# Kernel tuning notes

Measured on AMD Instinct MI355X. Metric: run time of the kernel, lower is better.

The kernel has to match this reference:

```python
import jax, jax.numpy as jnp
import numpy as np

N = 100000   # nodes
E = 1600000  # edges
S = 4        # state_dimension
H = 64       # hidden_channels


def _gcn_conv(x, row, col, W, b):
    """PyG GCNConv: h = x @ W; add self-loops; symmetric deg^-1/2 norm; scatter-add; + bias."""
    n = x.shape[0]
    h = x @ W  # [N, out]
    loop = jnp.arange(n, dtype=row.dtype)
    r = jnp.concatenate([row, loop])  # sources (with self-loops)
    c = jnp.concatenate([col, loop])  # targets (with self-loops)
    deg = jax.ops.segment_sum(jnp.ones(r.shape[0], h.dtype), c, num_segments=n)
    dinv = jnp.where(deg > 0, jax.lax.rsqrt(deg), 0.0)
    norm = dinv[r] * dinv[c]                      # [E+N]
    msg = h[r] * norm[:, None]                    # gather + scale, [E+N, out]
    out = jax.ops.segment_sum(msg, c, num_segments=n)  # scatter-add
    return out + b


def setup_inputs() -> dict:
    key = jax.random.key(0)
    k1, k2, k3, k4 = jax.random.split(key, 4)
    x = jax.random.normal(k1, (N, S), dtype=jnp.float32)
    edge_index = jax.random.randint(k2, (2, E), 0, N, dtype=jnp.int32)
    # Glorot-ish init for the two GCNConv linear layers (+ zero bias, PyG default)
    W1 = jax.random.normal(k3, (S, H), dtype=jnp.float32) * (1.0 / np.sqrt(S))
    b1 = jnp.zeros((H,), jnp.float32)
    W2 = jax.random.normal(k4, (H, S), dtype=jnp.float32) * (1.0 / np.sqrt(H))
    b2 = jnp.zeros((S,), jnp.float32)
    return {"x": x, "edge_index": edge_index, "W1": W1, "b1": b1, "W2": W2, "b2": b2}


def reference(x, edge_index, W1, b1, W2, b2):
    row, col = edge_index[0], edge_index[1]
    h = _gcn_conv(x, row, col, W1, b1)
    h = jax.nn.relu(h)
    out = _gcn_conv(h, row, col, W2, b2)
    return out
```

## Files before the change

### kernel.cpp

```cpp
#include <hip/hip_runtime.h>


#define CSHIFT  10
#define CNODES  1024
#define EPB     4096
#define PTH     512
#define PERBLK  128
#define PBSHIFT 7
#define CAPC    18432
#define HCAP    9216
#define ANODES  128
#define ACAP    2432

__global__ void __launch_bounds__(PTH) k_part(
        const int* __restrict__ row, const int* __restrict__ col,
        int e, int Kc, int NB, int* __restrict__ cnt,
        unsigned* __restrict__ stripe) {
    __shared__ int cur[128];
    int t = threadIdx.x, bx = blockIdx.x;
    if (t < 128) cur[t] = 0;
    __syncthreads();
    int lo = bx * EPB;
    int cbuf[8], rbuf[8];
#pragma unroll
    for (int k = 0; k < 8; ++k) {
        int i = lo + t + k * PTH;
        if (i < e) { cbuf[k] = col[i]; rbuf[k] = row[i]; }
        else { cbuf[k] = -1; rbuf[k] = 0; }
    }
    size_t sbase = (size_t)bx * PERBLK;
    size_t bstride = (size_t)NB * PERBLK;
#pragma unroll
    for (int k = 0; k < 8; ++k) {
        int c = cbuf[k];
        if (c < 0) continue;
        int b = c >> CSHIFT;
        int j = atomicAdd(&cur[b], 1);
        if (j < PERBLK)
            stripe[(size_t)b * bstride + sbase + j] =
                ((unsigned)rbuf[k] << CSHIFT) | (unsigned)(c & (CNODES - 1));
    }
    __syncthreads();
    if (t < Kc) cnt[t * NB + bx] = min(cur[t], PERBLK);
}

__global__ void __launch_bounds__(1024) k_sortH(
        const int* __restrict__ cnt, const unsigned* __restrict__ stripe,
        unsigned* __restrict__ sortedg, int* __restrict__ rstart,
        int* __restrict__ mtot, const float4* __restrict__ x,
        float* __restrict__ dinv, float4* __restrict__ y, int n, int NB) {
    __shared__ int hist[CNODES];
    __shared__ int cur[512];
    __shared__ int cntl[512];
    __shared__ unsigned sorted[HCAP];
    __shared__ int wsum[16], wpre[16];
    __shared__ int lowsh, msh;
    int bh = blockIdx.x, b = bh >> 1, h = bh & 1;
    int t = threadIdx.x, lane = t & 63, wv = t >> 6;
    for (int i = t; i < NB; i += 1024) cntl[i] = cnt[b * NB + i];
    hist[t] = 0;
    __syncthreads();
    size_t s0 = (size_t)b * NB * PERBLK;
    int nslot4 = (NB * PERBLK) >> 2;
    const uint4* st4 = (const uint4*)(stripe + s0);
    for (int g = t; g < nslot4; g += 1024) {
        int slot = g << 2;
        int cb = cntl[slot >> PBSHIFT];
        int j = slot & (PERBLK - 1);
        if (j >= cb) continue;
        uint4 w = st4[g];
        atomicAdd(&hist[w.x & (CNODES - 1)], 1);
        if (j + 1 < cb) atomicAdd(&hist[w.y & (CNODES - 1)], 1);
        if (j + 2 < cb) atomicAdd(&hist[w.z & (CNODES - 1)], 1);
        if (j + 3 < cb) atomicAdd(&hist[w.w & (CNODES - 1)], 1);
    }
    __syncthreads();
    int hv = hist[t];
    int v = hv;
#pragma unroll
    for (int off = 1; off < 64; off <<= 1) {
        int u = __shfl_up(v, off);
        if (lane >= off) v += u;
    }
    if (lane == 63) wsum[wv] = v;
    __syncthreads();
    if (t < 16) {
        int s = 0;
        for (int i = 0; i < t; ++i) s += wsum[i];
        wpre[t] = s;
    }
    __syncthreads();
    int incl = v + wpre[wv];
    if (t == 511) lowsh = incl;
    if (t == 1023) msh = incl;
    __syncthreads();
    int st = incl - hv;
    int low = lowsh, m = msh;
    int base = h ? low : 0;
    if ((t >> 9) == h) {
        cur[t & 511] = st - base;
        rstart[(b << CSHIFT) + t] = b * CAPC + st;
        int node = (b << CSHIFT) + t;
        if (node < n) {
            float di = rsqrtf((float)hv + 1.0f);
            dinv[node] = di;
            float4 xv = x[node];
            y[node] = make_float4(xv.x * di, xv.y * di, xv.z * di, xv.w * di);
        }
    }
    if (t == 0 && h == 0) mtot[b] = m;
    __syncthreads();
    for (int g = t; g < nslot4; g += 1024) {
        int slot = g << 2;
        int cb = cntl[slot >> PBSHIFT];
        int j = slot & (PERBLK - 1);
        if (j >= cb) continue;
        uint4 w = st4[g];
        int l0 = w.x & (CNODES - 1);
        if ((l0 >> 9) == h) { int p = atomicAdd(&cur[l0 & 511], 1); if (p < HCAP) sorted[p] = w.x >> CSHIFT; }
        if (j + 1 < cb) { int l = w.y & (CNODES - 1);
            if ((l >> 9) == h) { int p = atomicAdd(&cur[l & 511], 1); if (p < HCAP) sorted[p] = w.y >> CSHIFT; } }
        if (j + 2 < cb) { int l = w.z & (CNODES - 1);
            if ((l >> 9) == h) { int p = atomicAdd(&cur[l & 511], 1); if (p < HCAP) sorted[p] = w.z >> CSHIFT; } }
        if (j + 3 < cb) { int l = w.w & (CNODES - 1);
            if ((l >> 9) == h) { int p = atomicAdd(&cur[l & 511], 1); if (p < HCAP) sorted[p] = w.w >> CSHIFT; } }
    }
    __syncthreads();
    int cown = h ? (m - low) : low;
    int wb = min(cown, HCAP);
    size_t d0 = (size_t)b * CAPC + base;
    for (int i = t; i < wb; i += 1024) sortedg[d0 + i] = sorted[i];
}

__global__ void __launch_bounds__(512) k_mid(
        const unsigned* __restrict__ ere, const int* __restrict__ rstart,
        const int* __restrict__ mtot, const float* __restrict__ dinv,
        const float4* __restrict__ x, const float4* __restrict__ y,
        const float* __restrict__ W1, const float* __restrict__ b1,
        const float* __restrict__ W2, const float* __restrict__ b2,
        float4* __restrict__ z, float4* __restrict__ out, int n) {
    __shared__ unsigned recs[ACAP];
    __shared__ float4 sums[ANODES];
    int g = blockIdx.x, t = threadIdx.x;
    int nlo = g * ANODES;
    int b = nlo >> CSHIFT;
    int s0 = rstart[nlo];
    int e0 = ((g & 7) == 7) ? b * CAPC + min(mtot[b], CAPC)
                            : rstart[nlo + ANODES];
    int len = min(e0 - s0, ACAP);
    for (int i = t; i < len; i += 512) recs[i] = ere[s0 + i];
    __syncthreads();
    int tt = t >> 2, q = t & 3;
    int s = rstart[nlo + tt] - s0;
    int epos = (tt == ANODES - 1) ? len : min(rstart[nlo + tt + 1] - s0, len);
    float vx = 0.f, vy = 0.f, vz = 0.f, vw = 0.f;
    int i = s + q;
    while (i + 12 < epos) {
        int r0 = recs[i], r1 = recs[i + 4], r2 = recs[i + 8], r3 = recs[i + 12];
        float4 a0 = y[r0], a1 = y[r1], a2 = y[r2], a3 = y[r3];
        vx += a0.x + a1.x + a2.x + a3.x;
        vy += a0.y + a1.y + a2.y + a3.y;
        vz += a0.z + a1.z + a2.z + a3.z;
        vw += a0.w + a1.w + a2.w + a3.w;
        i += 16;
    }
    for (; i < epos; i += 4) {
        float4 a = y[recs[i]];
        vx += a.x; vy += a.y; vz += a.z; vw += a.w;
    }
    vx += __shfl_xor(vx, 1); vx += __shfl_xor(vx, 2);
    vy += __shfl_xor(vy, 1); vy += __shfl_xor(vy, 2);
    vz += __shfl_xor(vz, 1); vz += __shfl_xor(vz, 2);
    vw += __shfl_xor(vw, 1); vw += __shfl_xor(vw, 2);
    if (q == 0) sums[tt] = make_float4(vx, vy, vz, vw);
    __syncthreads();
    int node = nlo + t;
    if (t < ANODES && node < n) {
        float di = dinv[node], sl = di * di;
        float4 sv = sums[t];
        float4 xv = x[node];
        float a0 = di * sv.x + xv.x * sl;
        float a1 = di * sv.y + xv.y * sl;
        float a2 = di * sv.z + xv.z * sl;
        float a3 = di * sv.w + xv.w * sl;
        float t0 = 0.f, t1 = 0.f, t2 = 0.f, t3 = 0.f;
#pragma unroll 8
        for (int j = 0; j < 64; ++j) {
            float hh = b1[j] + a0 * W1[j] + a1 * W1[64 + j] + a2 * W1[128 + j] + a3 * W1[192 + j];
            hh = fmaxf(hh, 0.f);
            t0 += hh * W2[j * 4 + 0];
            t1 += hh * W2[j * 4 + 1];
            t2 += hh * W2[j * 4 + 2];
            t3 += hh * W2[j * 4 + 3];
        }
        z[node] = make_float4(t0 * di, t1 * di, t2 * di, t3 * di);
        out[node] = make_float4(b2[0] + t0 * sl, b2[1] + t1 * sl,
                                b2[2] + t2 * sl, b2[3] + t3 * sl);
    }
}

__global__ void __launch_bounds__(512) k_acc2(
        const unsigned* __restrict__ ere, const int* __restrict__ rstart,
        const int* __restrict__ mtot, const float* __restrict__ dinv,
        const float4* __restrict__ z, float4* __restrict__ out, int n) {
    __shared__ unsigned recs[ACAP];
    __shared__ float4 sums[ANODES];
    int g = blockIdx.x, t = threadIdx.x;
    int nlo = g * ANODES;
    int b = nlo >> CSHIFT;
    int s0 = rstart[nlo];
    int e0 = ((g & 7) == 7) ? b * CAPC + min(mtot[b], CAPC)
                            : rstart[nlo + ANODES];
    int len = min(e0 - s0, ACAP);
    for (int i = t; i < len; i += 512) recs[i] = ere[s0 + i];
    __syncthreads();
    int tt = t >> 2, q = t & 3;
    int s = rstart[nlo + tt] - s0;
    int epos = (tt == ANODES - 1) ? len : min(rstart[nlo + tt + 1] - s0, len);
    float vx = 0.f, vy = 0.f, vz = 0.f, vw = 0.f;
    int i = s + q;
    while (i + 12 < epos) {
        int r0 = recs[i], r1 = recs[i + 4], r2 = recs[i + 8], r3 = recs[i + 12];
        float4 a0 = z[r0], a1 = z[r1], a2 = z[r2], a3 = z[r3];
        vx += a0.x + a1.x + a2.x + a3.x;
        vy += a0.y + a1.y + a2.y + a3.y;
        vz += a0.z + a1.z + a2.z + a3.z;
        vw += a0.w + a1.w + a2.w + a3.w;
        i += 16;
    }
    for (; i < epos; i += 4) {
        float4 a = z[recs[i]];
        vx += a.x; vy += a.y; vz += a.z; vw += a.w;
    }
    vx += __shfl_xor(vx, 1); vx += __shfl_xor(vx, 2);
    vy += __shfl_xor(vy, 1); vy += __shfl_xor(vy, 2);
    vz += __shfl_xor(vz, 1); vz += __shfl_xor(vz, 2);
    vw += __shfl_xor(vw, 1); vw += __shfl_xor(vw, 2);
    if (q == 0) sums[tt] = make_float4(vx, vy, vz, vw);
    __syncthreads();
    int node = nlo + t;
    if (t < ANODES && node < n) {
        float di = dinv[node];
        float4 sv = sums[t];
        float4 o = out[node];
        out[node] = make_float4(o.x + di * sv.x, o.y + di * sv.y,
                                o.z + di * sv.z, o.w + di * sv.w);
    }
}

extern "C" void kernel_launch(void* const* d_in, const int* in_sizes, int n_in,
                              void* d_out, int out_size, void* d_ws, size_t ws_size,
                              hipStream_t stream) {
    const float* x  = (const float*)d_in[0];
    const int* edge = (const int*)d_in[1];
    const float* W1 = (const float*)d_in[2];
    const float* b1 = (const float*)d_in[3];
    const float* W2 = (const float*)d_in[4];
    const float* b2 = (const float*)d_in[5];
    float* out = (float*)d_out;

    const int n = in_sizes[0] / 4;
    const int e = in_sizes[1] / 2;
    const int* row = edge;
    const int* col = edge + e;
    const int Kc = (n + CNODES - 1) >> CSHIFT;
    const int NB = (e + EPB - 1) / EPB;

    char* ws = (char*)d_ws;
    float* y    = (float*)ws;  ws += (size_t)4 * n * 4;
    float* zmid = (float*)ws;  ws += (size_t)4 * n * 4;
    float* dinv = (float*)ws;  ws += (size_t)n * 4;
    unsigned* stripe = (unsigned*)ws;  ws += (size_t)Kc * NB * PERBLK * 4;
    unsigned* sortedg = (unsigned*)ws; ws += (size_t)Kc * CAPC * 4;
    int* cnt    = (int*)ws;    ws += (size_t)Kc * NB * 4;
    int* rstart = (int*)ws;    ws += (size_t)Kc * CNODES * 4;
    int* mtot   = (int*)ws;    ws += (size_t)Kc * 4;

    const int ga = (n + ANODES - 1) / ANODES;

    k_part<<<NB, PTH, 0, stream>>>(row, col, e, Kc, NB, cnt, stripe);
    k_sortH<<<2 * Kc, 1024, 0, stream>>>(cnt, stripe, sortedg, rstart, mtot,
                                         (const float4*)x, dinv, (float4*)y,
                                         n, NB);
    k_mid<<<ga, 512, 0, stream>>>(sortedg, rstart, mtot, dinv, (const float4*)x,
                                  (const float4*)y, W1, b1, W2, b2,
                                  (float4*)zmid, (float4*)out, n);
    k_acc2<<<ga, 512, 0, stream>>>(sortedg, rstart, mtot, dinv,
                                   (const float4*)zmid, (float4*)out, n);
}
```

Baseline: 125.7 us.

## Split sort into quarter-bucket blocks, per-wave partition histograms, direct global edge reads

The partition kernel now builds per-wave histograms and prefix offsets before scattering, which cuts contention on shared atomics. Each stripe segment shrinks to 96 slots. The sort kernel is split into four 512-thread blocks per 1024-node bucket instead of two 1024-thread blocks. This doubles the grid and shrinks shared memory per block, but every block still rescans the whole stripe. The aggregation kernels drop the shared-memory staging of edge records and read sorted indices straight from global memory, which removes a sync and the ACAP truncation. The risk is more redundant stripe reads and less coalesced index loads.

Measured after the change: 135.6 us. 7.9% more time.

```diff
diff --git a/kernel.cpp b/kernel.cpp
--- a/kernel.cpp
+++ b/kernel.cpp
@@ -5,20 +5,20 @@
 #define CNODES  1024
 #define EPB     4096
 #define PTH     512
-#define PERBLK  128
-#define PBSHIFT 7
+#define PERBLK  96
+#define QPS     24
 #define CAPC    18432
-#define HCAP    9216
+#define QCAP    4608
 #define ANODES  128
-#define ACAP    2432
+#define NBMAX   512
 
 __global__ void __launch_bounds__(PTH) k_part(
         const int* __restrict__ row, const int* __restrict__ col,
         int e, int Kc, int NB, int* __restrict__ cnt,
         unsigned* __restrict__ stripe) {
-    __shared__ int cur[128];
-    int t = threadIdx.x, bx = blockIdx.x;
-    if (t < 128) cur[t] = 0;
+    __shared__ int wh[8][128];
+    int t = threadIdx.x, w = t >> 6, bx = blockIdx.x;
+    for (int k = t; k < 8 * 128; k += PTH) ((int*)wh)[k] = 0;
     __syncthreads();
     int lo = bx * EPB;
     int cbuf[8], rbuf[8];
@@ -28,55 +28,69 @@
         if (i < e) { cbuf[k] = col[i]; rbuf[k] = row[i]; }
         else { cbuf[k] = -1; rbuf[k] = 0; }
     }
-    size_t sbase = (size_t)bx * PERBLK;
+#pragma unroll
+    for (int k = 0; k < 8; ++k)
+        if (cbuf[k] >= 0) atomicAdd(&wh[w][cbuf[k] >> CSHIFT], 1);
+    __syncthreads();
+    if (t < 128) {
+        int s = 0;
+#pragma unroll
+        for (int w2 = 0; w2 < 8; ++w2) s += wh[w2][t];
+        if (t < Kc) cnt[t * NB + bx] = min(s, PERBLK);
+        int run = 0;
+#pragma unroll
+        for (int w2 = 0; w2 < 8; ++w2) { int c = wh[w2][t]; wh[w2][t] = run; run += c; }
+    }
+    __syncthreads();
+    size_t segbase = (size_t)bx * PERBLK;
     size_t bstride = (size_t)NB * PERBLK;
 #pragma unroll
     for (int k = 0; k < 8; ++k) {
         int c = cbuf[k];
         if (c < 0) continue;
         int b = c >> CSHIFT;
-        int j = atomicAdd(&cur[b], 1);
+        int j = atomicAdd(&wh[w][b], 1);
         if (j < PERBLK)
-            stripe[(size_t)b * bstride + sbase + j] =
+            stripe[(size_t)b * bstride + segbase + j] =
                 ((unsigned)rbuf[k] << CSHIFT) | (unsigned)(c & (CNODES - 1));
     }
-    __syncthreads();
-    if (t < Kc) cnt[t * NB + bx] = min(cur[t], PERBLK);
-}
-
-__global__ void __launch_bounds__(1024) k_sortH(
+}
+
+__global__ void __launch_bounds__(512) k_sortQ(
         const int* __restrict__ cnt, const unsigned* __restrict__ stripe,
         unsigned* __restrict__ sortedg, int* __restrict__ rstart,
         int* __restrict__ mtot, const float4* __restrict__ x,
         float* __restrict__ dinv, float4* __restrict__ y, int n, int NB) {
     __shared__ int hist[CNODES];
-    __shared__ int cur[512];
-    __shared__ int cntl[512];
-    __shared__ unsigned sorted[HCAP];
-    __shared__ int wsum[16], wpre[16];
-    __shared__ int lowsh, msh;
-    int bh = blockIdx.x, b = bh >> 1, h = bh & 1;
+    __shared__ int scn[CNODES];
+    __shared__ int cur[256];
+    __shared__ int cntl[NBMAX];
+    __shared__ unsigned sorted[QCAP];
+    __shared__ int wsum[8];
+    __shared__ int bsh[5];
+    int bq = blockIdx.x, b = bq >> 2, h = bq & 3;
     int t = threadIdx.x, lane = t & 63, wv = t >> 6;
-    for (int i = t; i < NB; i += 1024) cntl[i] = cnt[b * NB + i];
-    hist[t] = 0;
+    for (int i = t; i < NB; i += 512) cntl[i] = cnt[b * NB + i];
+    hist[t] = 0; hist[t + 512] = 0;
     __syncthreads();
     size_t s0 = (size_t)b * NB * PERBLK;
-    int nslot4 = (NB * PERBLK) >> 2;
+    int nq = (NB * PERBLK) >> 2;
     const uint4* st4 = (const uint4*)(stripe + s0);
-    for (int g = t; g < nslot4; g += 1024) {
-        int slot = g << 2;
-        int cb = cntl[slot >> PBSHIFT];
-        int j = slot & (PERBLK - 1);
+    for (int g = t; g < nq; g += 512) {
+        int seg = g / QPS;
+        int j = (g - seg * QPS) << 2;
+        int cb = cntl[seg];
         if (j >= cb) continue;
-        uint4 w = st4[g];
-        atomicAdd(&hist[w.x & (CNODES - 1)], 1);
-        if (j + 1 < cb) atomicAdd(&hist[w.y & (CNODES - 1)], 1);
-        if (j + 2 < cb) atomicAdd(&hist[w.z & (CNODES - 1)], 1);
-        if (j + 3 < cb) atomicAdd(&hist[w.w & (CNODES - 1)], 1);
-    }
-    __syncthreads();
-    int hv = hist[t];
-    int v = hv;
+        uint4 wr = st4[g];
+        atomicAdd(&hist[wr.x & (CNODES - 1)], 1);
+        if (j + 1 < cb) atomicAdd(&hist[wr.y & (CNODES - 1)], 1);
+        if (j + 2 < cb) atomicAdd(&hist[wr.z & (CNODES - 1)], 1);
+        if (j + 3 < cb) atomicAdd(&hist[wr.w & (CNODES - 1)], 1);
+    }
+    __syncthreads();
+    int h0 = hist[2 * t], h1 = hist[2 * t + 1];
+    int s = h0 + h1;
+    int v = s;
 #pragma unroll
     for (int off = 1; off < 64; off <<= 1) {
         int u = __shfl_up(v, off);
@@ -84,52 +98,51 @@
     }
     if (lane == 63) wsum[wv] = v;
     __syncthreads();
-    if (t < 16) {
-        int s = 0;
-        for (int i = 0; i < t; ++i) s += wsum[i];
-        wpre[t] = s;
-    }
-    __syncthreads();
-    int incl = v + wpre[wv];
-    if (t == 511) lowsh = incl;
-    if (t == 1023) msh = incl;
-    __syncthreads();
-    int st = incl - hv;
-    int low = lowsh, m = msh;
-    int base = h ? low : 0;
-    if ((t >> 9) == h) {
-        cur[t & 511] = st - base;
-        rstart[(b << CSHIFT) + t] = b * CAPC + st;
-        int node = (b << CSHIFT) + t;
+    int wpre = 0;
+    for (int i = 0; i < wv; ++i) wpre += wsum[i];
+    int incl = v + wpre;
+    scn[2 * t] = incl - s;
+    scn[2 * t + 1] = incl - h1;
+    if (t == 0) bsh[0] = 0;
+    if (t == 127) bsh[1] = incl;
+    if (t == 255) bsh[2] = incl;
+    if (t == 383) bsh[3] = incl;
+    if (t == 511) bsh[4] = incl;
+    __syncthreads();
+    int m = bsh[4], base = bsh[h], qend = bsh[h + 1];
+    if (t < 256) {
+        int bin = (h << 8) + t;
+        cur[t] = scn[bin] - base;
+        rstart[(b << CSHIFT) + bin] = b * CAPC + scn[bin];
+        int node = (b << CSHIFT) + bin;
         if (node < n) {
-            float di = rsqrtf((float)hv + 1.0f);
+            float di = rsqrtf((float)hist[bin] + 1.0f);
             dinv[node] = di;
             float4 xv = x[node];
             y[node] = make_float4(xv.x * di, xv.y * di, xv.z * di, xv.w * di);
         }
     }
-    if (t == 0 && h == 0) mtot[b] = m;
-    __syncthreads();
-    for (int g = t; g < nslot4; g += 1024) {
-        int slot = g << 2;
-        int cb = cntl[slot >> PBSHIFT];
-        int j = slot & (PERBLK - 1);
+    if (h == 0 && t == 0) mtot[b] = m;
+    __syncthreads();
+    for (int g = t; g < nq; g += 512) {
+        int seg = g / QPS;
+        int j = (g - seg * QPS) << 2;
+        int cb = cntl[seg];
         if (j >= cb) continue;
-        uint4 w = st4[g];
-        int l0 = w.x & (CNODES - 1);
-        if ((l0 >> 9) == h) { int p = atomicAdd(&cur[l0 & 511], 1); if (p < HCAP) sorted[p] = w.x >> CSHIFT; }
-        if (j + 1 < cb) { int l = w.y & (CNODES - 1);
-            if ((l >> 9) == h) { int p = atomicAdd(&cur[l & 511], 1); if (p < HCAP) sorted[p] = w.y >> CSHIFT; } }
-        if (j + 2 < cb) { int l = w.z & (CNODES - 1);
-            if ((l >> 9) == h) { int p = atomicAdd(&cur[l & 511], 1); if (p < HCAP) sorted[p] = w.z >> CSHIFT; } }
-        if (j + 3 < cb) { int l = w.w & (CNODES - 1);
-            if ((l >> 9) == h) { int p = atomicAdd(&cur[l & 511], 1); if (p < HCAP) sorted[p] = w.w >> CSHIFT; } }
-    }
-    __syncthreads();
-    int cown = h ? (m - low) : low;
-    int wb = min(cown, HCAP);
+        uint4 wr = st4[g];
+        int l0 = wr.x & (CNODES - 1);
+        if ((l0 >> 8) == h) { int p = atomicAdd(&cur[l0 & 255], 1); if (p < QCAP) sorted[p] = wr.x >> CSHIFT; }
+        if (j + 1 < cb) { int l = wr.y & (CNODES - 1);
+            if ((l >> 8) == h) { int p = atomicAdd(&cur[l & 255], 1); if (p < QCAP) sorted[p] = wr.y >> CSHIFT; } }
+        if (j + 2 < cb) { int l = wr.z & (CNODES - 1);
+            if ((l >> 8) == h) { int p = atomicAdd(&cur[l & 255], 1); if (p < QCAP) sorted[p] = wr.z >> CSHIFT; } }
+        if (j + 3 < cb) { int l = wr.w & (CNODES - 1);
+            if ((l >> 8) == h) { int p = atomicAdd(&cur[l & 255], 1); if (p < QCAP) sorted[p] = wr.w >> CSHIFT; } }
+    }
+    __syncthreads();
+    int wb = min(qend - base, QCAP);
     size_t d0 = (size_t)b * CAPC + base;
-    for (int i = t; i < wb; i += 1024) sortedg[d0 + i] = sorted[i];
+    for (int i = t; i < wb; i += 512) sortedg[d0 + i] = sorted[i];
 }
 
 __global__ void __launch_bounds__(512) k_mid(
@@ -139,24 +152,19 @@
         const float* __restrict__ W1, const float* __restrict__ b1,
         const float* __restrict__ W2, const float* __restrict__ b2,
         float4* __restrict__ z, float4* __restrict__ out, int n) {
-    __shared__ unsigned recs[ACAP];
     __shared__ float4 sums[ANODES];
     int g = blockIdx.x, t = threadIdx.x;
     int nlo = g * ANODES;
     int b = nlo >> CSHIFT;
-    int s0 = rstart[nlo];
-    int e0 = ((g & 7) == 7) ? b * CAPC + min(mtot[b], CAPC)
-                            : rstart[nlo + ANODES];
-    int len = min(e0 - s0, ACAP);
-    for (int i = t; i < len; i += 512) recs[i] = ere[s0 + i];
-    __syncthreads();
     int tt = t >> 2, q = t & 3;
-    int s = rstart[nlo + tt] - s0;
-    int epos = (tt == ANODES - 1) ? len : min(rstart[nlo + tt + 1] - s0, len);
+    int sA = rstart[nlo + tt];
+    int eA = (tt == ANODES - 1)
+        ? (((g & 7) == 7) ? b * CAPC + min(mtot[b], CAPC) : rstart[nlo + ANODES])
+        : rstart[nlo + tt + 1];
     float vx = 0.f, vy = 0.f, vz = 0.f, vw = 0.f;
-    int i = s + q;
-    while (i + 12 < epos) {
-        int r0 = recs[i], r1 = recs[i + 4], r2 = recs[i + 8], r3 = recs[i + 12];
+    int i = sA + q;
+    while (i + 12 < eA) {
+        int r0 = ere[i], r1 = ere[i + 4], r2 = ere[i + 8], r3 = ere[i + 12];
         float4 a0 = y[r0], a1 = y[r1], a2 = y[r2], a3 = y[r3];
         vx += a0.x + a1.x + a2.x + a3.x;
         vy += a0.y + a1.y + a2.y + a3.y;
@@ -164,8 +172,8 @@
         vw += a0.w + a1.w + a2.w + a3.w;
         i += 16;
     }
-    for (; i < epos; i += 4) {
-        float4 a = y[recs[i]];
+    for (; i < eA; i += 4) {
+        float4 a = y[ere[i]];
         vx += a.x; vy += a.y; vz += a.z; vw += a.w;
     }
     vx += __shfl_xor(vx, 1); vx += __shfl_xor(vx, 2);
@@ -203,24 +211,19 @@
         const unsigned* __restrict__ ere, const int* __restrict__ rstart,
         const int* __restrict__ mtot, const float* __restrict__ dinv,
         const float4* __restrict__ z, float4* __restrict__ out, int n) {
-    __shared__ unsigned recs[ACAP];
     __shared__ float4 sums[ANODES];
     int g = blockIdx.x, t = threadIdx.x;
     int nlo = g * ANODES;
     int b = nlo >> CSHIFT;
-    int s0 = rstart[nlo];
-    int e0 = ((g & 7) == 7) ? b * CAPC + min(mtot[b], CAPC)
-                            : rstart[nlo + ANODES];
-    int len = min(e0 - s0, ACAP);
-    for (int i = t; i < len; i += 512) recs[i] = ere[s0 + i];
-    __syncthreads();
     int tt = t >> 2, q = t & 3;
-    int s = rstart[nlo + tt] - s0;
-    int epos = (tt == ANODES - 1) ? len : min(rstart[nlo + tt + 1] - s0, len);
+    int sA = rstart[nlo + tt];
+    int eA = (tt == ANODES - 1)
+        ? (((g & 7) == 7) ? b * CAPC + min(mtot[b], CAPC) : rstart[nlo + ANODES])
+        : rstart[nlo + tt + 1];
     float vx = 0.f, vy = 0.f, vz = 0.f, vw = 0.f;
-    int i = s + q;
-    while (i + 12 < epos) {
-        int r0 = recs[i], r1 = recs[i + 4], r2 = recs[i + 8], r3 = recs[i + 12];
+    int i = sA + q;
+    while (i + 12 < eA) {
+        int r0 = ere[i], r1 = ere[i + 4], r2 = ere[i + 8], r3 = ere[i + 12];
         float4 a0 = z[r0], a1 = z[r1], a2 = z[r2], a3 = z[r3];
         vx += a0.x + a1.x + a2.x + a3.x;
         vy += a0.y + a1.y + a2.y + a3.y;
@@ -228,8 +231,8 @@
         vw += a0.w + a1.w + a2.w + a3.w;
         i += 16;
     }
-    for (; i < epos; i += 4) {
-        float4 a = z[recs[i]];
+    for (; i < eA; i += 4) {
+        float4 a = z[ere[i]];
         vx += a.x; vy += a.y; vz += a.z; vw += a.w;
     }
     vx += __shfl_xor(vx, 1); vx += __shfl_xor(vx, 2);
@@ -279,9 +282,9 @@
     const int ga = (n + ANODES - 1) / ANODES;
 
     k_part<<<NB, PTH, 0, stream>>>(row, col, e, Kc, NB, cnt, stripe);
-    k_sortH<<<2 * Kc, 1024, 0, stream>>>(cnt, stripe, sortedg, rstart, mtot,
-                                         (const float4*)x, dinv, (float4*)y,
-                                         n, NB);
+    k_sortQ<<<4 * Kc, 512, 0, stream>>>(cnt, stripe, sortedg, rstart, mtot,
+                                        (const float4*)x, dinv, (float4*)y,
+                                        n, NB);
     k_mid<<<ga, 512, 0, stream>>>(sortedg, rstart, mtot, dinv, (const float4*)x,
                                   (const float4*)y, W1, b1, W2, b2,
                                   (float4*)zmid, (float4*)out, n);
```
